# Kernel tuning notes

Measured on AMD Instinct MI355X. Metric: run time of the kernel, lower is better.

## Reference

```python
import jax, jax.numpy as jnp
import numpy as np

M, N, D, P = 16, 2048, 128, 8192
H = N // D  # 16
MAXLEN = 8448
EPS = 1e-5


def layernorm(x, g, b):
    mu = jnp.mean(x, axis=-1, keepdims=True)
    var = jnp.mean(jnp.square(x - mu), axis=-1, keepdims=True)
    return (x - mu) * jax.lax.rsqrt(var + EPS) * g + b


def setup_inputs() -> dict:
    key = jax.random.key(0)
    ks = jax.random.split(key, 10)
    s = 1.0 / np.sqrt(N)  # keep activations O(1) like trained weights
    return {
        "X": jax.random.normal(ks[0], (M, N), jnp.float32),
        "ln1_g": jnp.ones((N,), jnp.float32),
        "ln1_b": jnp.zeros((N,), jnp.float32),
        "Wq": jax.random.normal(ks[1], (N, N), jnp.float32) * s,
        "Wk": jax.random.normal(ks[2], (N, N), jnp.float32) * s,
        "Wv": jax.random.normal(ks[3], (N, N), jnp.float32) * s,
        "Wo": jax.random.normal(ks[4], (N, N), jnp.float32) * s,
        "ln2_g": jnp.ones((N,), jnp.float32),
        "ln2_b": jnp.zeros((N,), jnp.float32),
        "Wup": jax.random.normal(ks[5], (4 * N, N), jnp.float32) * s,
        "Wdown": jax.random.normal(ks[6], (N, 4 * N), jnp.float32) * (1.0 / np.sqrt(4 * N)),
        "cache_K": jax.random.normal(ks[7], (H, MAXLEN, D), jnp.float32),
        "cache_V": jax.random.normal(ks[8], (H, MAXLEN, D), jnp.float32),
    }


def reference(X, ln1_g, ln1_b, Wq, Wk, Wv, Wo, ln2_g, ln2_b, Wup, Wdown, cache_K, cache_V):
    residual = X
    Xn = layernorm(X, ln1_g, ln1_b)
    # torch Linear: y = x @ W.T
    q = (Xn @ Wq.T).reshape(M, H, D).transpose(1, 0, 2)  # (H,M,D)
    k = (Xn @ Wk.T).reshape(M, H, D).transpose(1, 0, 2)
    v = (Xn @ Wv.T).reshape(M, H, D).transpose(1, 0, 2)
    # KV-cache append
    cache_K = jax.lax.dynamic_update_slice(cache_K, k, (0, P, 0))
    cache_V = jax.lax.dynamic_update_slice(cache_V, v, (0, P, 0))
    Kc = cache_K[:, : P + M, :]  # (H,T,D), T = P+M
    Vc = cache_V[:, : P + M, :]
    scores = jnp.einsum("hmd,htd->hmt", q, Kc) / np.sqrt(D)
    weights = jax.nn.softmax(scores, axis=-1)
    attn = jnp.einsum("hmt,htd->hmd", weights, Vc)  # (H,M,D)
    attn = attn.transpose(1, 0, 2).reshape(M, N)
    X = residual + attn @ Wo.T
    residual = X
    Xn = layernorm(X, ln2_g, ln2_b)
    ffn = jax.nn.gelu(Xn @ Wup.T, approximate=False) @ Wdown.T
    return residual + ffn
```

## Files before the change

### kernel.cpp

```cpp
#include <hip/hip_runtime.h>
#include <hip/hip_bf16.h>
#include <math.h>

#define M_TOK 16
#define NDIM  2048
#define DHEAD 128
#define NHEAD 16
#define MAXLEN 8448
#define FFN   8192
#define TC    128
#define NCH   65
#define LN_EPS 1e-5f
#define RSQRT_D 0.08838834764831845f

#define AS1 __attribute__((address_space(1)))
#define AS3 __attribute__((address_space(3)))

__device__ __forceinline__ void gload_lds16(const float* g, float* l) {
    __builtin_amdgcn_global_load_lds((AS1 void*)g, (AS3 void*)l, 16, 0, 0);
}

template<int H>
__device__ __forceinline__ void fold_step(float* v, int lane, int o) {
    bool hi = (lane & o) != 0;
    #pragma unroll
    for (int i = 0; i < H; ++i) {
        float send = hi ? v[i] : v[i + H];
        float keep = hi ? v[i + H] : v[i];
        v[i] = keep + __shfl_xor(send, o);
    }
}

__device__ __forceinline__ void fold16(float* v, int lane) {
    fold_step<8>(v, lane, 32);
    fold_step<4>(v, lane, 16);
    fold_step<2>(v, lane, 8);
    fold_step<1>(v, lane, 4);
    v[0] += __shfl_xor(v[0], 2);
    v[0] += __shfl_xor(v[0], 1);
}

template<int KDIM>
__device__ __forceinline__ void gemv_core16(const float* __restrict__ A,
                                            const float* __restrict__ W,
                                            int cb, int w, int lane,
                                            float* sbuf, float* acc) {
    constexpr int NS = KDIM / 256;
    const float* wsrc = W + (size_t)(cb + w) * KDIM + lane * 4;
    auto issue = [&](int s) {
        if (s >= NS) return;
        float* dst = sbuf + (s & 1) * 5120;
        gload_lds16(wsrc + s * 256, dst + w * 256);
        #pragma unroll
        for (int j = 0; j < 4; ++j) {
            int m = w * 4 + j;
            gload_lds16(A + (size_t)m * KDIM + s * 256 + lane * 4,
                        dst + 1024 + m * 256);
        }
    };
    issue(0);
    issue(1);
    #pragma unroll 1
    for (int s = 0; s < NS; ++s) {
        if (s == NS - 1) asm volatile("s_waitcnt vmcnt(0) lgkmcnt(0)" ::: "memory");
        else             asm volatile("s_waitcnt vmcnt(5) lgkmcnt(0)" ::: "memory");
        __builtin_amdgcn_s_barrier();
        const float* buf = sbuf + (s & 1) * 5120;
        float4 wr[4], xr[4];
        #pragma unroll
        for (int c = 0; c < 4; ++c)
            wr[c] = *(const float4*)(buf + c * 256 + lane * 4);
        #pragma unroll
        for (int j = 0; j < 4; ++j)
            xr[j] = *(const float4*)(buf + 1024 + (w * 4 + j) * 256 + lane * 4);
        asm volatile("s_waitcnt lgkmcnt(0)" ::: "memory");
        __builtin_amdgcn_s_barrier();
        issue(s + 2);
        #pragma unroll
        for (int j = 0; j < 4; ++j) {
            #pragma unroll
            for (int c = 0; c < 4; ++c) {
                acc[j*4+c] = fmaf(wr[c].x, xr[j].x, acc[j*4+c]);
                acc[j*4+c] = fmaf(wr[c].y, xr[j].y, acc[j*4+c]);
                acc[j*4+c] = fmaf(wr[c].z, xr[j].z, acc[j*4+c]);
                acc[j*4+c] = fmaf(wr[c].w, xr[j].w, acc[j*4+c]);
            }
        }
    }
}

__global__ __launch_bounds__(256) void k_qkv(const float* __restrict__ Xn,
                                             const float* __restrict__ Wq,
                                             const float* __restrict__ Wk,
                                             const float* __restrict__ Wv,
                                             float* __restrict__ qws,
                                             float* __restrict__ kws,
                                             float* __restrict__ vws) {
    __shared__ float sbuf[2 * 5120];
    int tid = threadIdx.x, w = tid >> 6, lane = tid & 63;
    int b = blockIdx.x;
    int sel = b >> 9;
    int cb = (b & 511) * 4;
    const float* W = (sel == 0) ? Wq : (sel == 1) ? Wk : Wv;
    float* dst = (sel == 0) ? qws : (sel == 1) ? kws : vws;
    float acc[16];
    #pragma unroll
    for (int i = 0; i < 16; ++i) acc[i] = 0.f;
    gemv_core16<2048>(Xn, W, cb, w, lane, sbuf, acc);
    fold16(acc, lane);
    if ((lane & 3) == 0) {
        int idx = lane >> 2;
        int j = idx >> 2, c = idx & 3;
        int m = w * 4 + j;
        int gcol = cb + c;
        int hh = gcol >> 7, d = gcol & 127;
        dst[(((size_t)hh * 16 + m) << 7) + d] = acc[0];
    }
}

__device__ __forceinline__ float gelu_exact(float x) {
    return 0.5f * x * (1.0f + erff(x * 0.7071067811865475f));
}

__global__ __launch_bounds__(256) void k_up(const float* __restrict__ A,
                                            const float* __restrict__ W,
                                            float* __restrict__ out) {
    __shared__ float sbuf[2 * 5120];
    int tid = threadIdx.x, w = tid >> 6, lane = tid & 63;
    int cb = blockIdx.x * 4;
    float acc[16];
    #pragma unroll
    for (int i = 0; i < 16; ++i) acc[i] = 0.f;
    gemv_core16<2048>(A, W, cb, w, lane, sbuf, acc);
    fold16(acc, lane);
    if ((lane & 3) == 0) {
        int idx = lane >> 2;
        int j = idx >> 2, c = idx & 3;
        int m = w * 4 + j;
        out[(size_t)m * FFN + cb + c] = gelu_exact(acc[0]);
    }
}

template<int KDIM>
__global__ __launch_bounds__(256) void k_resid(const float* __restrict__ A,
                                               const float* __restrict__ W,
                                               const float* __restrict__ R,
                                               float* __restrict__ out) {
    __shared__ float sbuf[2 * 5120];
    int tid = threadIdx.x, w = tid >> 6, lane = tid & 63;
    int cb = blockIdx.x * 4;
    float acc[16];
    #pragma unroll
    for (int i = 0; i < 16; ++i) acc[i] = 0.f;
    gemv_core16<KDIM>(A, W, cb, w, lane, sbuf, acc);
    fold16(acc, lane);
    if ((lane & 3) == 0) {
        int idx = lane >> 2;
        int j = idx >> 2, c = idx & 3;
        int m = w * 4 + j;
        int col = cb + c;
        out[(size_t)m * NDIM + col] = R[(size_t)m * NDIM + col] + acc[0];
    }
}

__global__ __launch_bounds__(256) void k_ln(const float* __restrict__ X,
                                            const float* __restrict__ g,
                                            const float* __restrict__ b,
                                            float* __restrict__ out) {
    int row = blockIdx.x, tid = threadIdx.x;
    const float4* xp = (const float4*)(X + (size_t)row * NDIM);
    float4 v0 = xp[tid], v1 = xp[tid + 256];
    float s = v0.x + v0.y + v0.z + v0.w + v1.x + v1.y + v1.z + v1.w;
    float q = v0.x*v0.x + v0.y*v0.y + v0.z*v0.z + v0.w*v0.w
            + v1.x*v1.x + v1.y*v1.y + v1.z*v1.z + v1.w*v1.w;
    #pragma unroll
    for (int o = 32; o; o >>= 1) { s += __shfl_xor(s, o); q += __shfl_xor(q, o); }
    __shared__ float ls[4], lq[4];
    int wid = tid >> 6, lane = tid & 63;
    if (lane == 0) { ls[wid] = s; lq[wid] = q; }
    __syncthreads();
    s = ls[0] + ls[1] + ls[2] + ls[3];
    q = lq[0] + lq[1] + lq[2] + lq[3];
    float mu  = s * (1.f / NDIM);
    float var = q * (1.f / NDIM) - mu * mu;
    float rs  = rsqrtf(var + LN_EPS);
    float4 g0 = ((const float4*)g)[tid], g1 = ((const float4*)g)[tid + 256];
    float4 b0 = ((const float4*)b)[tid], b1 = ((const float4*)b)[tid + 256];
    float4 o0, o1;
    o0.x = (v0.x - mu) * rs * g0.x + b0.x;  o0.y = (v0.y - mu) * rs * g0.y + b0.y;
    o0.z = (v0.z - mu) * rs * g0.z + b0.z;  o0.w = (v0.w - mu) * rs * g0.w + b0.w;
    o1.x = (v1.x - mu) * rs * g1.x + b1.x;  o1.y = (v1.y - mu) * rs * g1.y + b1.y;
    o1.z = (v1.z - mu) * rs * g1.z + b1.z;  o1.w = (v1.w - mu) * rs * g1.w + b1.w;
    float4* op = (float4*)(out + (size_t)row * NDIM);
    op[tid] = o0; op[tid + 256] = o1;
}

__global__ __launch_bounds__(256, 2) void k_attn(const float* __restrict__ cacheK,
                                                 const float* __restrict__ cacheV,
                                                 const float* __restrict__ qws,
                                                 const float* __restrict__ kws,
                                                 const float* __restrict__ vws,
                                                 float* __restrict__ part,
                                                 float* __restrict__ ms) {
    __shared__ float s_k[2][2080];
    __shared__ float s_v[2][2080];
    __shared__ float s_p[16][132];
    int bid = blockIdx.x;
    int h = bid / NCH, c = bid % NCH;
    int nT = (c < NCH - 1) ? TC : M_TOK;
    int NST = nT >> 4;
    const float* Kb = (c < NCH - 1) ? cacheK + ((size_t)h * MAXLEN + (size_t)c * TC) * DHEAD
                                    : kws + (size_t)h * M_TOK * DHEAD;
    const float* Vb = (c < NCH - 1) ? cacheV + ((size_t)h * MAXLEN + (size_t)c * TC) * DHEAD
                                    : vws + (size_t)h * M_TOK * DHEAD;
    int tid = threadIdx.x, w = tid >> 6, lane = tid & 63;
    int tloc = lane & 15, ds = lane >> 4;

    float4 qreg[4][8];
    {
        const float4* qp = (const float4*)(qws + (size_t)h * M_TOK * DHEAD);
        #pragma unroll
        for (int mm = 0; mm < 4; ++mm) {
            #pragma unroll
            for (int i = 0; i < 8; ++i)
                qreg[mm][i] = qp[(size_t)(w * 4 + mm) * 32 + ds * 8 + i];
        }
    }
    asm volatile("s_waitcnt vmcnt(0)" ::: "memory");

    auto issue = [&](int slot) {
        if (slot >= 2 * NST) return;
        const float* src; float* dst;
        if (slot < NST) { src = Kb + (size_t)slot * 16 * DHEAD; dst = s_k[slot & 1]; }
        else { int j = slot - NST; src = Vb + (size_t)j * 16 * DHEAD; dst = s_v[j & 1]; }
        #pragma unroll
        for (int k = 0; k < 2; ++k) {
            int j = w * 2 + k;
            gload_lds16(src + j * 256 + lane * 4, dst + j * 260);
        }
    };

    issue(0);
    issue(1);
    const int lastSlot = 2 * NST - 1;

    for (int s = 0; s < NST; ++s) {
        if (s == lastSlot) asm volatile("s_waitcnt vmcnt(0) lgkmcnt(0)" ::: "memory");
        else               asm volatile("s_waitcnt vmcnt(2) lgkmcnt(0)" ::: "memory");
        __builtin_amdgcn_s_barrier();
        const float* kbase = s_k[s & 1] + (tloc >> 1) * 260 + (tloc & 1) * 128 + ds * 32;
        float4 kr[8];
        #pragma unroll
        for (int i = 0; i < 8; ++i) kr[i] = *(const float4*)(kbase + i * 4);
        asm volatile("s_waitcnt lgkmcnt(0)" ::: "memory");
        __builtin_amdgcn_s_barrier();
        issue(s + 2);
        #pragma unroll
        for (int mm = 0; mm < 4; ++mm) {
            float a0 = 0.f, a1 = 0.f, a2 = 0.f, a3 = 0.f;
            #pragma unroll
            for (int i = 0; i < 8; ++i) {
                a0 = fmaf(kr[i].x, qreg[mm][i].x, a0);
                a1 = fmaf(kr[i].y, qreg[mm][i].y, a1);
                a2 = fmaf(kr[i].z, qreg[mm][i].z, a2);
                a3 = fmaf(kr[i].w, qreg[mm][i].w, a3);
            }
            float s0 = (a0 + a1) + (a2 + a3);
            s0 += __shfl_xor(s0, 16);
            s0 += __shfl_xor(s0, 32);
            if (ds == 0) s_p[w * 4 + mm][s * 16 + tloc] = s0 * RSQRT_D;
        }
    }

    asm volatile("s_waitcnt lgkmcnt(0)" ::: "memory");
    __builtin_amdgcn_s_barrier();
    {
        int m2 = tid >> 4, tl = tid & 15;
        float mx = -1e30f;
        for (int t = tl; t < nT; t += 16) mx = fmaxf(mx, s_p[m2][t]);
        #pragma unroll
        for (int o = 8; o; o >>= 1) mx = fmaxf(mx, __shfl_xor(mx, o));
        float sm = 0.f;
        for (int t = tl; t < nT; t += 16) {
            float p = __expf(s_p[m2][t] - mx);
            s_p[m2][t] = p;
            sm += p;
        }
        #pragma unroll
        for (int o = 8; o; o >>= 1) sm += __shfl_xor(sm, o);
        if (tl == 0) {
            float* msp = ms + ((size_t)(h * NCH + c) * 16 + m2) * 2;
            msp[0] = mx; msp[1] = sm;
        }
    }

    float2 acc[4] = {{0.f,0.f},{0.f,0.f},{0.f,0.f},{0.f,0.f}};
    for (int j = 0; j < NST; ++j) {
        int s = NST + j;
        if (s == lastSlot) asm volatile("s_waitcnt vmcnt(0) lgkmcnt(0)" ::: "memory");
        else               asm volatile("s_waitcnt vmcnt(2) lgkmcnt(0)" ::: "memory");
        __builtin_amdgcn_s_barrier();
        float2 vr[16];
        const float* vbase = s_v[j & 1];
        #pragma unroll
        for (int r = 0; r < 16; ++r)
            vr[r] = *(const float2*)(vbase + (r >> 1) * 260 + (r & 1) * 128 + lane * 2);
        asm volatile("s_waitcnt lgkmcnt(0)" ::: "memory");
        __builtin_amdgcn_s_barrier();
        issue(s + 2);
        #pragma unroll
        for (int mm = 0; mm < 4; ++mm) {
            int m = w * 4 + mm;
            const float* prow = &s_p[m][j * 16];
            #pragma unroll
            for (int g4 = 0; g4 < 4; ++g4) {
                float4 p4 = *(const float4*)(prow + g4 * 4);
                acc[mm].x = fmaf(p4.x, vr[g4*4+0].x, acc[mm].x);
                acc[mm].y = fmaf(p4.x, vr[g4*4+0].y, acc[mm].y);
                acc[mm].x = fmaf(p4.y, vr[g4*4+1].x, acc[mm].x);
                acc[mm].y = fmaf(p4.y, vr[g4*4+1].y, acc[mm].y);
                acc[mm].x = fmaf(p4.z, vr[g4*4+2].x, acc[mm].x);
                acc[mm].y = fmaf(p4.z, vr[g4*4+2].y, acc[mm].y);
                acc[mm].x = fmaf(p4.w, vr[g4*4+3].x, acc[mm].x);
                acc[mm].y = fmaf(p4.w, vr[g4*4+3].y, acc[mm].y);
            }
        }
    }

    float* dp = part + (((size_t)(h * NCH + c) * 16) + w * 4) * DHEAD + 2 * lane;
    #pragma unroll
    for (int mm = 0; mm < 4; ++mm)
        *(float2*)(dp + (size_t)mm * DHEAD) = acc[mm];
}

__global__ __launch_bounds__(256) void k_combine(const float* __restrict__ part,
                                                 const float* __restrict__ ms,
                                                 float* __restrict__ attnout) {
    __shared__ float s_scale[16][NCH + 3];
    int h = blockIdx.x >> 3, dblk = blockIdx.x & 7;
    int tid = threadIdx.x;
    {
        int cl = tid & 15, m = tid >> 4;
        float gmax = -1e30f;
        for (int c = cl; c < NCH; c += 16)
            gmax = fmaxf(gmax, ms[((size_t)(h * NCH + c) * 16 + m) * 2]);
        #pragma unroll
        for (int o = 8; o; o >>= 1) gmax = fmaxf(gmax, __shfl_xor(gmax, o));
        float denom = 0.f;
        for (int c = cl; c < NCH; c += 16) {
            const float* msp = ms + ((size_t)(h * NCH + c) * 16 + m) * 2;
            denom += msp[1] * __expf(msp[0] - gmax);
        }
        #pragma unroll
        for (int o = 8; o; o >>= 1) denom += __shfl_xor(denom, o);
        float inv = 1.f / denom;
        for (int c = cl; c < NCH; c += 16) {
            const float* msp = ms + ((size_t)(h * NCH + c) * 16 + m) * 2;
            s_scale[m][c] = __expf(msp[0] - gmax) * inv;
        }
    }
    __syncthreads();
    int m = tid >> 4, dd = tid & 15;
    int d = dblk * 16 + dd;
    const float* pp = part + ((size_t)h * NCH * 16 + m) * DHEAD + d;
    float acc = 0.f;
    #pragma unroll 4
    for (int c = 0; c < NCH; ++c)
        acc = fmaf(pp[(size_t)c * 16 * DHEAD], s_scale[m][c], acc);
    attnout[(size_t)m * NDIM + h * DHEAD + d] = acc;
}

extern "C" void kernel_launch(void* const* d_in, const int* in_sizes, int n_in,
                              void* d_out, int out_size, void* d_ws, size_t ws_size,
                              hipStream_t stream) {
    const float* X      = (const float*)d_in[0];
    const float* ln1_g  = (const float*)d_in[1];
    const float* ln1_b  = (const float*)d_in[2];
    const float* Wq     = (const float*)d_in[3];
    const float* Wk     = (const float*)d_in[4];
    const float* Wv     = (const float*)d_in[5];
    const float* Wo     = (const float*)d_in[6];
    const float* ln2_g  = (const float*)d_in[7];
    const float* ln2_b  = (const float*)d_in[8];
    const float* Wup    = (const float*)d_in[9];
    const float* Wdown  = (const float*)d_in[10];
    const float* cacheK = (const float*)d_in[11];
    const float* cacheV = (const float*)d_in[12];
    float* out = (float*)d_out;

    float* ws = (float*)d_ws;
    float* Xn1    = ws;
    float* qws    = Xn1 + 32768;
    float* kws    = qws + 32768;
    float* vws    = kws + 32768;
    float* partb  = vws + 32768;
    float* msb    = partb + 2129920;
    float* attn_o = msb + 33280;
    float* X2     = attn_o + 32768;
    float* Xn2    = X2 + 32768;
    float* ffnh   = Xn2 + 32768;

    k_ln<<<M_TOK, 256, 0, stream>>>(X, ln1_g, ln1_b, Xn1);
    k_qkv<<<1536, 256, 0, stream>>>(Xn1, Wq, Wk, Wv, qws, kws, vws);
    k_attn<<<NHEAD * NCH, 256, 0, stream>>>(cacheK, cacheV, qws, kws, vws, partb, msb);
    k_combine<<<NHEAD * 8, 256, 0, stream>>>(partb, msb, attn_o);
    k_resid<2048><<<512, 256, 0, stream>>>(attn_o, Wo, X, X2);
    k_ln<<<M_TOK, 256, 0, stream>>>(X2, ln2_g, ln2_b, Xn2);
    k_up<<<2048, 256, 0, stream>>>(Xn2, Wup, ffnh);
    k_resid<8192><<<512, 256, 0, stream>>>(ffnh, Wdown, X2, out);
}
```

Measured before the change: 144.6 us.

## Widen GEMV tiles to eight columns and deepen LDS prefetch pipelines

The GEMV core now computes 8 weight rows per block instead of 4, with each wave owning two rows across all 16 tokens. Its LDS ring grows from double to triple buffering, and grid sizes are halved to match. The attention kernel's K/V staging goes from 2 to 4 buffers with a graded vmcnt wait ladder. The aim is to keep more global loads in flight and reuse activations across more weight rows, at the cost of more LDS, more registers and fewer blocks for the Wo and Wdown projections.

```diff
diff --git a/kernel.cpp b/kernel.cpp
--- a/kernel.cpp
+++ b/kernel.cpp
@@ -31,60 +31,63 @@
     }
 }
 
-__device__ __forceinline__ void fold16(float* v, int lane) {
-    fold_step<8>(v, lane, 32);
-    fold_step<4>(v, lane, 16);
-    fold_step<2>(v, lane, 8);
-    fold_step<1>(v, lane, 4);
-    v[0] += __shfl_xor(v[0], 2);
+__device__ __forceinline__ void fold32(float* v, int lane) {
+    fold_step<16>(v, lane, 32);
+    fold_step<8>(v, lane, 16);
+    fold_step<4>(v, lane, 8);
+    fold_step<2>(v, lane, 4);
+    fold_step<1>(v, lane, 2);
     v[0] += __shfl_xor(v[0], 1);
 }
 
 template<int KDIM>
-__device__ __forceinline__ void gemv_core16(const float* __restrict__ A,
-                                            const float* __restrict__ W,
-                                            int cb, int w, int lane,
-                                            float* sbuf, float* acc) {
+__device__ __forceinline__ void gemv_core8(const float* __restrict__ A,
+                                           const float* __restrict__ W,
+                                           int cb, int w, int lane,
+                                           float* sbuf, float* acc) {
     constexpr int NS = KDIM / 256;
-    const float* wsrc = W + (size_t)(cb + w) * KDIM + lane * 4;
+    const float* wsrc0 = W + (size_t)(cb + 2 * w)     * KDIM + lane * 4;
+    const float* wsrc1 = W + (size_t)(cb + 2 * w + 1) * KDIM + lane * 4;
     auto issue = [&](int s) {
         if (s >= NS) return;
-        float* dst = sbuf + (s & 1) * 5120;
-        gload_lds16(wsrc + s * 256, dst + w * 256);
+        float* dst = sbuf + (s % 3) * 6144;
+        gload_lds16(wsrc0 + s * 256, dst + (2 * w) * 256);
+        gload_lds16(wsrc1 + s * 256, dst + (2 * w + 1) * 256);
         #pragma unroll
         for (int j = 0; j < 4; ++j) {
             int m = w * 4 + j;
             gload_lds16(A + (size_t)m * KDIM + s * 256 + lane * 4,
-                        dst + 1024 + m * 256);
+                        dst + 2048 + m * 256);
         }
     };
-    issue(0);
-    issue(1);
+    issue(0); issue(1); issue(2);
     #pragma unroll 1
     for (int s = 0; s < NS; ++s) {
-        if (s == NS - 1) asm volatile("s_waitcnt vmcnt(0) lgkmcnt(0)" ::: "memory");
-        else             asm volatile("s_waitcnt vmcnt(5) lgkmcnt(0)" ::: "memory");
-        __builtin_amdgcn_s_barrier();
-        const float* buf = sbuf + (s & 1) * 5120;
-        float4 wr[4], xr[4];
-        #pragma unroll
-        for (int c = 0; c < 4; ++c)
-            wr[c] = *(const float4*)(buf + c * 256 + lane * 4);
-        #pragma unroll
-        for (int j = 0; j < 4; ++j)
-            xr[j] = *(const float4*)(buf + 1024 + (w * 4 + j) * 256 + lane * 4);
+        int rem = NS - 1 - s;
+        if (rem >= 2)      asm volatile("s_waitcnt vmcnt(12) lgkmcnt(0)" ::: "memory");
+        else if (rem == 1) asm volatile("s_waitcnt vmcnt(6) lgkmcnt(0)" ::: "memory");
+        else               asm volatile("s_waitcnt vmcnt(0) lgkmcnt(0)" ::: "memory");
+        __builtin_amdgcn_s_barrier();
+        const float* buf = sbuf + (s % 3) * 6144;
+        float4 wr0 = *(const float4*)(buf + (2 * w) * 256 + lane * 4);
+        float4 wr1 = *(const float4*)(buf + (2 * w + 1) * 256 + lane * 4);
+        float4 xr[16];
+        #pragma unroll
+        for (int m = 0; m < 16; ++m)
+            xr[m] = *(const float4*)(buf + 2048 + m * 256 + lane * 4);
         asm volatile("s_waitcnt lgkmcnt(0)" ::: "memory");
         __builtin_amdgcn_s_barrier();
-        issue(s + 2);
-        #pragma unroll
-        for (int j = 0; j < 4; ++j) {
-            #pragma unroll
-            for (int c = 0; c < 4; ++c) {
-                acc[j*4+c] = fmaf(wr[c].x, xr[j].x, acc[j*4+c]);
-                acc[j*4+c] = fmaf(wr[c].y, xr[j].y, acc[j*4+c]);
-                acc[j*4+c] = fmaf(wr[c].z, xr[j].z, acc[j*4+c]);
-                acc[j*4+c] = fmaf(wr[c].w, xr[j].w, acc[j*4+c]);
-            }
+        issue(s + 3);
+        #pragma unroll
+        for (int m = 0; m < 16; ++m) {
+            acc[m*2]   = fmaf(wr0.x, xr[m].x, acc[m*2]);
+            acc[m*2]   = fmaf(wr0.y, xr[m].y, acc[m*2]);
+            acc[m*2]   = fmaf(wr0.z, xr[m].z, acc[m*2]);
+            acc[m*2]   = fmaf(wr0.w, xr[m].w, acc[m*2]);
+            acc[m*2+1] = fmaf(wr1.x, xr[m].x, acc[m*2+1]);
+            acc[m*2+1] = fmaf(wr1.y, xr[m].y, acc[m*2+1]);
+            acc[m*2+1] = fmaf(wr1.z, xr[m].z, acc[m*2+1]);
+            acc[m*2+1] = fmaf(wr1.w, xr[m].w, acc[m*2+1]);
         }
     }
 }
@@ -96,23 +99,22 @@
                                              float* __restrict__ qws,
                                              float* __restrict__ kws,
                                              float* __restrict__ vws) {
-    __shared__ float sbuf[2 * 5120];
+    __shared__ float sbuf[3 * 6144];
     int tid = threadIdx.x, w = tid >> 6, lane = tid & 63;
     int b = blockIdx.x;
-    int sel = b >> 9;
-    int cb = (b & 511) * 4;
+    int sel = b >> 8;
+    int cb = (b & 255) * 8;
     const float* W = (sel == 0) ? Wq : (sel == 1) ? Wk : Wv;
     float* dst = (sel == 0) ? qws : (sel == 1) ? kws : vws;
-    float acc[16];
-    #pragma unroll
-    for (int i = 0; i < 16; ++i) acc[i] = 0.f;
-    gemv_core16<2048>(Xn, W, cb, w, lane, sbuf, acc);
-    fold16(acc, lane);
-    if ((lane & 3) == 0) {
-        int idx = lane >> 2;
-        int j = idx >> 2, c = idx & 3;
-        int m = w * 4 + j;
-        int gcol = cb + c;
+    float acc[32];
+    #pragma unroll
+    for (int i = 0; i < 32; ++i) acc[i] = 0.f;
+    gemv_core8<2048>(Xn, W, cb, w, lane, sbuf, acc);
+    fold32(acc, lane);
+    if ((lane & 1) == 0) {
+        int idx = (lane >> 1) & 31;
+        int m = idx >> 1, c = idx & 1;
+        int gcol = cb + 2 * w + c;
         int hh = gcol >> 7, d = gcol & 127;
         dst[(((size_t)hh * 16 + m) << 7) + d] = acc[0];
     }
@@ -125,19 +127,18 @@
 __global__ __launch_bounds__(256) void k_up(const float* __restrict__ A,
                                             const float* __restrict__ W,
                                             float* __restrict__ out) {
-    __shared__ float sbuf[2 * 5120];
+    __shared__ float sbuf[3 * 6144];
     int tid = threadIdx.x, w = tid >> 6, lane = tid & 63;
-    int cb = blockIdx.x * 4;
-    float acc[16];
-    #pragma unroll
-    for (int i = 0; i < 16; ++i) acc[i] = 0.f;
-    gemv_core16<2048>(A, W, cb, w, lane, sbuf, acc);
-    fold16(acc, lane);
-    if ((lane & 3) == 0) {
-        int idx = lane >> 2;
-        int j = idx >> 2, c = idx & 3;
-        int m = w * 4 + j;
-        out[(size_t)m * FFN + cb + c] = gelu_exact(acc[0]);
+    int cb = blockIdx.x * 8;
+    float acc[32];
+    #pragma unroll
+    for (int i = 0; i < 32; ++i) acc[i] = 0.f;
+    gemv_core8<2048>(A, W, cb, w, lane, sbuf, acc);
+    fold32(acc, lane);
+    if ((lane & 1) == 0) {
+        int idx = (lane >> 1) & 31;
+        int m = idx >> 1, c = idx & 1;
+        out[(size_t)m * FFN + cb + 2 * w + c] = gelu_exact(acc[0]);
     }
 }
 
@@ -146,19 +147,18 @@
                                                const float* __restrict__ W,
                                                const float* __restrict__ R,
                                                float* __restrict__ out) {
-    __shared__ float sbuf[2 * 5120];
+    __shared__ float sbuf[3 * 6144];
     int tid = threadIdx.x, w = tid >> 6, lane = tid & 63;
-    int cb = blockIdx.x * 4;
-    float acc[16];
-    #pragma unroll
-    for (int i = 0; i < 16; ++i) acc[i] = 0.f;
-    gemv_core16<KDIM>(A, W, cb, w, lane, sbuf, acc);
-    fold16(acc, lane);
-    if ((lane & 3) == 0) {
-        int idx = lane >> 2;
-        int j = idx >> 2, c = idx & 3;
-        int m = w * 4 + j;
-        int col = cb + c;
+    int cb = blockIdx.x * 8;
+    float acc[32];
+    #pragma unroll
+    for (int i = 0; i < 32; ++i) acc[i] = 0.f;
+    gemv_core8<KDIM>(A, W, cb, w, lane, sbuf, acc);
+    fold32(acc, lane);
+    if ((lane & 1) == 0) {
+        int idx = (lane >> 1) & 31;
+        int m = idx >> 1, c = idx & 1;
+        int col = cb + 2 * w + c;
         out[(size_t)m * NDIM + col] = R[(size_t)m * NDIM + col] + acc[0];
     }
 }
@@ -202,8 +202,8 @@
                                                  const float* __restrict__ vws,
                                                  float* __restrict__ part,
                                                  float* __restrict__ ms) {
-    __shared__ float s_k[2][2080];
-    __shared__ float s_v[2][2080];
+    __shared__ float s_k[4][2080];
+    __shared__ float s_v[4][2080];
     __shared__ float s_p[16][132];
     int bid = blockIdx.x;
     int h = bid / NCH, c = bid % NCH;
@@ -231,8 +231,8 @@
     auto issue = [&](int slot) {
         if (slot >= 2 * NST) return;
         const float* src; float* dst;
-        if (slot < NST) { src = Kb + (size_t)slot * 16 * DHEAD; dst = s_k[slot & 1]; }
-        else { int j = slot - NST; src = Vb + (size_t)j * 16 * DHEAD; dst = s_v[j & 1]; }
+        if (slot < NST) { src = Kb + (size_t)slot * 16 * DHEAD; dst = s_k[slot & 3]; }
+        else { int j = slot - NST; src = Vb + (size_t)j * 16 * DHEAD; dst = s_v[j & 3]; }
         #pragma unroll
         for (int k = 0; k < 2; ++k) {
             int j = w * 2 + k;
@@ -240,21 +240,26 @@
         }
     };
 
-    issue(0);
-    issue(1);
+    issue(0); issue(1); issue(2); issue(3);
     const int lastSlot = 2 * NST - 1;
 
+    #define WAIT_LADDER(s)                                                          \
+        { int rem = lastSlot - (s);                                                 \
+          if (rem >= 3)      asm volatile("s_waitcnt vmcnt(6) lgkmcnt(0)" ::: "memory"); \
+          else if (rem == 2) asm volatile("s_waitcnt vmcnt(4) lgkmcnt(0)" ::: "memory"); \
+          else if (rem == 1) asm volatile("s_waitcnt vmcnt(2) lgkmcnt(0)" ::: "memory"); \
+          else               asm volatile("s_waitcnt vmcnt(0) lgkmcnt(0)" ::: "memory"); }
+
     for (int s = 0; s < NST; ++s) {
-        if (s == lastSlot) asm volatile("s_waitcnt vmcnt(0) lgkmcnt(0)" ::: "memory");
-        else               asm volatile("s_waitcnt vmcnt(2) lgkmcnt(0)" ::: "memory");
-        __builtin_amdgcn_s_barrier();
-        const float* kbase = s_k[s & 1] + (tloc >> 1) * 260 + (tloc & 1) * 128 + ds * 32;
+        WAIT_LADDER(s);
+        __builtin_amdgcn_s_barrier();
+        const float* kbase = s_k[s & 3] + (tloc >> 1) * 260 + (tloc & 1) * 128 + ds * 32;
         float4 kr[8];
         #pragma unroll
         for (int i = 0; i < 8; ++i) kr[i] = *(const float4*)(kbase + i * 4);
         asm volatile("s_waitcnt lgkmcnt(0)" ::: "memory");
         __builtin_amdgcn_s_barrier();
-        issue(s + 2);
+        issue(s + 4);
         #pragma unroll
         for (int mm = 0; mm < 4; ++mm) {
             float a0 = 0.f, a1 = 0.f, a2 = 0.f, a3 = 0.f;
@@ -272,8 +277,6 @@
         }
     }
 
-    asm volatile("s_waitcnt lgkmcnt(0)" ::: "memory");
-    __builtin_amdgcn_s_barrier();
     {
         int m2 = tid >> 4, tl = tid & 15;
         float mx = -1e30f;
@@ -297,17 +300,16 @@
     float2 acc[4] = {{0.f,0.f},{0.f,0.f},{0.f,0.f},{0.f,0.f}};
     for (int j = 0; j < NST; ++j) {
         int s = NST + j;
-        if (s == lastSlot) asm volatile("s_waitcnt vmcnt(0) lgkmcnt(0)" ::: "memory");
-        else               asm volatile("s_waitcnt vmcnt(2) lgkmcnt(0)" ::: "memory");
+        WAIT_LADDER(s);
         __builtin_amdgcn_s_barrier();
         float2 vr[16];
-        const float* vbase = s_v[j & 1];
+        const float* vbase = s_v[j & 3];
         #pragma unroll
         for (int r = 0; r < 16; ++r)
             vr[r] = *(const float2*)(vbase + (r >> 1) * 260 + (r & 1) * 128 + lane * 2);
         asm volatile("s_waitcnt lgkmcnt(0)" ::: "memory");
         __builtin_amdgcn_s_barrier();
-        issue(s + 2);
+        issue(s + 4);
         #pragma unroll
         for (int mm = 0; mm < 4; ++mm) {
             int m = w * 4 + mm;
@@ -326,6 +328,7 @@
             }
         }
     }
+    #undef WAIT_LADDER
 
     float* dp = part + (((size_t)(h * NCH + c) * 16) + w * 4) * DHEAD + 2 * lane;
     #pragma unroll
@@ -401,11 +404,11 @@
     float* ffnh   = Xn2 + 32768;
 
     k_ln<<<M_TOK, 256, 0, stream>>>(X, ln1_g, ln1_b, Xn1);
-    k_qkv<<<1536, 256, 0, stream>>>(Xn1, Wq, Wk, Wv, qws, kws, vws);
+    k_qkv<<<768, 256, 0, stream>>>(Xn1, Wq, Wk, Wv, qws, kws, vws);
     k_attn<<<NHEAD * NCH, 256, 0, stream>>>(cacheK, cacheV, qws, kws, vws, partb, msb);
     k_combine<<<NHEAD * 8, 256, 0, stream>>>(partb, msb, attn_o);
-    k_resid<2048><<<512, 256, 0, stream>>>(attn_o, Wo, X, X2);
+    k_resid<2048><<<256, 256, 0, stream>>>(attn_o, Wo, X, X2);
     k_ln<<<M_TOK, 256, 0, stream>>>(X2, ln2_g, ln2_b, Xn2);
-    k_up<<<2048, 256, 0, stream>>>(Xn2, Wup, ffnh);
-    k_resid<8192><<<512, 256, 0, stream>>>(ffnh, Wdown, X2, out);
-}
+    k_up<<<1024, 256, 0, stream>>>(Xn2, Wup, ffnh);
+    k_resid<8192><<<256, 256, 0, stream>>>(ffnh, Wdown, X2, out);
+}
```

Measured after the change: 145.0 us. Within noise of the previous version (+0.3%).
